# Performance work log

Hardware: AMD Instinct MI355X
Metric: run time of the kernel (lower is better)

Reference implementation:

```python
import jax, jax.numpy as jnp
import numpy as np

T, N, E = 12, 2048, 32768
X_DIM, H_DIM, Z_DIM, NL = 128, 256, 32, 2
EPS = 1e-10


def setup_inputs() -> dict:
    key = jax.random.key(0)
    ks = jax.random.split(key, 24)
    s = 0.1  # reset_parameters stdv
    p = {}
    p['x'] = jax.random.normal(ks[0], (T, N, X_DIM), jnp.float32)
    p['edge_index'] = jax.random.randint(ks[1], (T, 2, E), 0, N, dtype=jnp.int32)
    p['adj'] = (jax.random.uniform(ks[2], (T, N, N)) < 0.01).astype(jnp.float32)
    p['eps_src'] = jax.random.normal(ks[3], (T, N, Z_DIM), jnp.float32)
    p['eps_dst'] = jax.random.normal(ks[4], (T, N, Z_DIM), jnp.float32)
    p['phi_x_w'] = s * jax.random.normal(ks[5], (X_DIM, H_DIM), jnp.float32)
    p['phi_z_w'] = s * jax.random.normal(ks[6], (2 * Z_DIM, H_DIM), jnp.float32)
    p['gru_xw0'] = s * jax.random.normal(ks[7], (3, 2 * H_DIM, H_DIM), jnp.float32)  # (z,r,h) layer 0
    p['gru_xw1'] = s * jax.random.normal(ks[8], (3, H_DIM, H_DIM), jnp.float32)      # (z,r,h) layer 1
    p['gru_hw'] = s * jax.random.normal(ks[9], (NL, 3, H_DIM, H_DIM), jnp.float32)
    p['enc_w'] = s * jax.random.normal(ks[10], (2, 2 * H_DIM, H_DIM), jnp.float32)   # [src,dst]
    p['enc_b'] = s * jax.random.normal(ks[11], (2, H_DIM), jnp.float32)
    p['mean_w'] = s * jax.random.normal(ks[12], (2, H_DIM, Z_DIM), jnp.float32)
    p['mean_b'] = s * jax.random.normal(ks[13], (2, Z_DIM), jnp.float32)
    p['std_w'] = s * jax.random.normal(ks[14], (2, H_DIM, Z_DIM), jnp.float32)
    p['std_b'] = s * jax.random.normal(ks[15], (2, Z_DIM), jnp.float32)
    p['pri_w'] = s * jax.random.normal(ks[16], (2, H_DIM, H_DIM), jnp.float32)
    p['pri_b'] = s * jax.random.normal(ks[17], (2, H_DIM), jnp.float32)
    p['pri_mw'] = s * jax.random.normal(ks[18], (2, H_DIM, Z_DIM), jnp.float32)
    p['pri_mb'] = s * jax.random.normal(ks[19], (2, Z_DIM), jnp.float32)
    p['pri_sw'] = s * jax.random.normal(ks[20], (2, H_DIM, Z_DIM), jnp.float32)
    p['pri_sb'] = s * jax.random.normal(ks[21], (2, Z_DIM), jnp.float32)
    return p


def _gin_pre(x, src, dst):
    # GIN (eps=0): x + sum_{(src->dst)} x[src]; linear applied by caller
    return x + jax.ops.segment_sum(x[src], dst, num_segments=N)


def _gcn(x, w, b, src, dst):
    # GCNConv with self-loops and symmetric normalization
    deg = jax.ops.segment_sum(jnp.ones(src.shape[0], x.dtype), dst, num_segments=N) + 1.0
    dinv = deg ** -0.5
    nrm = dinv[src] * dinv[dst]
    xw = x @ w
    agg = jax.ops.segment_sum(nrm[:, None] * xw[src], dst, num_segments=N)
    return agg + xw / deg[:, None] + b


def _kld(m1, s1, m2, s2):
    k = (2 * jnp.log(s2 + EPS) - 2 * jnp.log(s1 + EPS)
         + ((s1 + EPS) ** 2 + (m1 - m2) ** 2) / (s2 + EPS) ** 2 - 1.0)
    return 0.5 / N * jnp.mean(jnp.sum(k, axis=1))


def reference(x, edge_index, adj, eps_src, eps_dst, phi_x_w, phi_z_w,
              gru_xw0, gru_xw1, gru_hw, enc_w, enc_b, mean_w, mean_b,
              std_w, std_b, pri_w, pri_b, pri_mw, pri_mb, pri_sw, pri_sb):
    h0 = jnp.zeros((NL, N, H_DIM), x.dtype)

    def step(h, inp):
        x_t, e_t, a_t, es_t, ed_t = inp
        src, dst = e_t[0], e_t[1]
        phi_x_t = jax.nn.relu(x_t @ phi_x_w)
        cat = jnp.concatenate([phi_x_t, h[-1]], axis=1)  # [N, 2H]
        cat_pre = _gin_pre(cat, src, dst)
        enc_s = jax.nn.relu(cat_pre @ enc_w[0] + enc_b[0])
        enc_d = jax.nn.relu(cat_pre @ enc_w[1] + enc_b[1])
        mean_s = _gcn(enc_s, mean_w[0], mean_b[0], src, dst)
        std_s = jax.nn.softplus(_gin_pre(enc_s, src, dst) @ std_w[0] + std_b[0])
        mean_d = _gcn(enc_d, mean_w[1], mean_b[1], src, dst)
        std_d = jax.nn.softplus(_gin_pre(enc_d, src, dst) @ std_w[1] + std_b[1])
        pri_s = jax.nn.relu(h[-1] @ pri_w[0] + pri_b[0])
        pm_s = pri_s @ pri_mw[0] + pri_mb[0]
        ps_s = jax.nn.softplus(pri_s @ pri_sw[0] + pri_sb[0])
        pri_d = jax.nn.relu(h[-1] @ pri_w[1] + pri_b[1])
        pm_d = pri_d @ pri_mw[1] + pri_mb[1]
        ps_d = jax.nn.softplus(pri_d @ pri_sw[1] + pri_sb[1])
        z_s = mean_s + std_s * es_t
        z_d = mean_d + std_d * ed_t
        phi_z_t = jax.nn.relu(jnp.concatenate([z_s, z_d], axis=1) @ phi_z_w)
        dec = z_s @ z_d.T  # [N, N] inner-product decoder (identity act)
        # graph-GRU across layers
        g_in = jnp.concatenate([phi_x_t, phi_z_t], axis=1)  # [N, 2H]
        new_h = []
        for i in range(NL):
            xi = g_in if i == 0 else new_h[i - 1]
            xw = gru_xw0 if i == 0 else gru_xw1
            xpre = _gin_pre(xi, src, dst)
            hpre = _gin_pre(h[i], src, dst)
            z_g = jax.nn.sigmoid(xpre @ xw[0] + hpre @ gru_hw[i, 0])
            r_g = jax.nn.sigmoid(xpre @ xw[1] + hpre @ gru_hw[i, 1])
            h_t = jnp.tanh(xpre @ xw[2] + _gin_pre(r_g * h[i], src, dst) @ gru_hw[i, 2])
            new_h.append(z_g * h[i] + (1.0 - z_g) * h_t)
        h_new = jnp.stack(new_h)
        kld = _kld(mean_s, std_s, pm_s, ps_s) + _kld(mean_d, std_d, pm_d, ps_d)
        ssum = a_t.sum()
        nn2 = jnp.asarray(N * N, a_t.dtype)
        posw = (nn2 - ssum) / ssum
        norm = nn2 / ((nn2 - ssum) * 2.0)
        bce = -posw * a_t * jax.nn.log_sigmoid(dec) - (1.0 - a_t) * jax.nn.log_sigmoid(-dec)
        nll = norm * jnp.mean(bce)
        return h_new, (kld, nll, dec)

    _, (klds, nlls, decs) = jax.lax.scan(step, h0, (x, edge_index, adj, eps_src, eps_dst))
    return jnp.sum(klds), jnp.sum(nlls), decs
```

## Files before the change

### kernel.cpp

```cpp
#include <hip/hip_runtime.h>
#include <math.h>

#define NTS 12
#define NND 2048
#define NED 32768
#define XDI 128
#define HDI 256
#define ZDI 32
#define EPSC 1e-10f
#define NH ((size_t)NND * HDI)
#define NZ ((size_t)NND * ZDI)
#define ZPL ((size_t)NND * 64)
#define XSZ ((size_t)NTS * NND * XDI)

typedef unsigned short u16;
typedef __bf16 bf16x8 __attribute__((ext_vector_type(8)));
typedef float f32x4 __attribute__((ext_vector_type(4)));

#define MF(a, b, c) __builtin_amdgcn_mfma_f32_16x16x32_bf16(a, b, c, 0, 0, 0)


__device__ __forceinline__ float lsigf(float x) {
    return fminf(x, 0.f) - log1pf(expf(-fabsf(x)));
}
__device__ __forceinline__ float splus(float v) {
    return fmaxf(v, 0.f) + log1pf(expf(-fabsf(v)));
}
__device__ __forceinline__ u16 f2b(float f) {
    unsigned u = __float_as_uint(f);
    u += 0x7fffu + ((u >> 16) & 1u);
    return (u16)(u >> 16);
}
__device__ __forceinline__ float b2f(u16 b) {
    return __uint_as_float((unsigned)b << 16);
}
__device__ __forceinline__ void f2b2(float v, u16& hi, u16& lo) {
    hi = f2b(v);
    lo = f2b(v - b2f(hi));
}
__device__ __forceinline__ void st_b16(u16* buf, size_t plane, size_t idx, float v) {
    u16 hi, lo;
    f2b2(v, hi, lo);
    buf[idx] = hi;
    buf[plane + idx] = lo;
}
__device__ __forceinline__ void st_b16v4(u16* buf, size_t plane, size_t idx, float4 v) {
    ushort4 h, l;
    f2b2(v.x, h.x, l.x); f2b2(v.y, h.y, l.y);
    f2b2(v.z, h.z, l.z); f2b2(v.w, h.w, l.w);
    *(ushort4*)(buf + idx) = h;
    *(ushort4*)(buf + plane + idx) = l;
}
__device__ __forceinline__ float4 ld_hl4(const u16* b, size_t plane, size_t idx) {
    ushort4 h = *(const ushort4*)(b + idx);
    ushort4 l = *(const ushort4*)(b + plane + idx);
    float4 r;
    r.x = b2f(h.x) + b2f(l.x); r.y = b2f(h.y) + b2f(l.y);
    r.z = b2f(h.z) + b2f(l.z); r.w = b2f(h.w) + b2f(l.w);
    return r;
}
__device__ float4 gin_hl(const u16* buf, size_t plane, int n, const int* __restrict__ offs,
                         const int* __restrict__ cs, int lane) {
    int e0 = offs[n], e1 = offs[n + 1];
    size_t c4 = (size_t)lane * 4;
    float4 a = ld_hl4(buf, plane, (size_t)n * HDI + c4);
    for (int j = e0; j < e1; j++) {
        float4 v = ld_hl4(buf, plane, (size_t)cs[j] * HDI + c4);
        a.x += v.x; a.y += v.y; a.z += v.z; a.w += v.w;
    }
    return a;
}

__host__ __device__ inline size_t wtoff(int m) {
    if (m == 0) return 0;
    if (m == 1) return 65536;
    return 98304 + (size_t)(m - 2) * 131072;
}

__device__ __forceinline__ void mm64(f32x4* A12, const u16* __restrict__ Ahi, size_t apl,
                                     const u16* __restrict__ Bt, int K,
                                     int row0, int cc, int lr, int kg) {
    const u16* bp = Bt + (size_t)(cc * 16 + lr) * K + kg;
    const u16* blp = bp + (size_t)K * HDI;
    const u16* ap0 = Ahi + (size_t)(row0 + lr) * K + kg;
    for (int k0 = 0; k0 < K; k0 += 32) {
        bf16x8 bh = *(const bf16x8*)(bp + k0);
        bf16x8 bl = *(const bf16x8*)(blp + k0);
#pragma unroll
        for (int s = 0; s < 4; s++) {
            const u16* ap = ap0 + (size_t)(16 * s) * K;
            bf16x8 ah = *(const bf16x8*)(ap + k0);
            bf16x8 al = *(const bf16x8*)(ap + apl + k0);
            A12[s * 3 + 0] = MF(ah, bh, A12[s * 3 + 0]);
            A12[s * 3 + 1] = MF(al, bh, A12[s * 3 + 1]);
            A12[s * 3 + 2] = MF(ah, bl, A12[s * 3 + 2]);
        }
    }
}

__device__ __forceinline__ void epi_hl(f32x4* A12, u16* dst, size_t plane,
                                       int row0, int cc, int lane, int relu) {
    int col = cc * 16 + (lane & 15);
    int rb0 = (lane >> 4) << 2;
#pragma unroll
    for (int s = 0; s < 4; s++)
#pragma unroll
        for (int i = 0; i < 4; i++) {
            int row = row0 + s * 16 + rb0 + i;
            float v = A12[s * 3][i] + A12[s * 3 + 1][i] + A12[s * 3 + 2][i];
            if (relu) v = fmaxf(v, 0.f);
            st_b16(dst, plane, (size_t)row * HDI + col, v);
        }
}


__global__ __launch_bounds__(256) void k0_setup(const int* __restrict__ ei,
                                                const float* __restrict__ x,
                                                const float* w_phix, const float* w_phiz,
                                                const float* w_enc, const float* w_pri,
                                                const float* w_gx0, const float* w_gx1,
                                                const float* w_gh,
                                                u16* __restrict__ warena, u16* __restrict__ xb,
                                                int* __restrict__ counts) {
    const int bid = blockIdx.x, tid = threadIdx.x;
    if (bid < 1536) {
        int idx = bid * 256 + tid;
        int t = idx >> 15, e = idx & (NED - 1);
        atomicAdd(&counts[t * NND + ei[(size_t)t * 2 * NED + NED + e]], 1);
    } else if (bid < 7424) {
        int u = bid - 1536;
        int m = u >> 8, k = u & 255;
        const int Kt = (m == 0) ? 128 : (m == 1) ? 64 : 256;
        if (k < Kt) {
            const int srcsel[23] = {0, 1, 2, 2, 2, 2, 3, 3, 4, 4, 4, 4,
                                    4, 4, 6, 6, 6, 5, 5, 5, 6, 6, 6};
            const int srcoff[23] = {0, 0, 0, 65536, 131072, 196608, 0, 65536,
                                    0, 65536, 131072, 196608, 262144, 327680,
                                    0, 65536, 131072, 0, 65536, 131072,
                                    196608, 262144, 327680};
            const float* srcs[7] = {w_phix, w_phiz, w_enc, w_pri, w_gx0, w_gx1, w_gh};
            const float* W = srcs[srcsel[m]] + srcoff[m];
            u16* D = warena + wtoff(m);
            float v = W[(size_t)k * 256 + tid];
            u16 hi, lo;
            f2b2(v, hi, lo);
            D[(size_t)tid * Kt + k] = hi;
            D[(size_t)Kt * 256 + (size_t)tid * Kt + k] = lo;
        }
    } else {
        size_t i = (size_t)(bid - 7424) * 256 + tid;
        float4 v = ((const float4*)x)[i];
        ushort4 h, l;
        f2b2(v.x, h.x, l.x); f2b2(v.y, h.y, l.y);
        f2b2(v.z, h.z, l.z); f2b2(v.w, h.w, l.w);
        ((ushort4*)xb)[i] = h;
        ((ushort4*)(xb + XSZ))[i] = l;
    }
}

__global__ __launch_bounds__(256) void k1_scan_phix(const int* __restrict__ counts,
                                                    int* __restrict__ offs,
                                                    float* __restrict__ deg,
                                                    float* __restrict__ dinv,
                                                    const u16* __restrict__ xb,
                                                    const u16* __restrict__ warena,
                                                    u16* __restrict__ phixb) {
    __shared__ int tsum[256];
    const int bid = blockIdx.x, tid = threadIdx.x;
    if (bid < 12) {
        const int* cnt = counts + bid * NND;
        int* off = offs + bid * (NND + 1);
        float* dg = deg + bid * NND;
        float* dv = dinv + bid * NND;
        int base = tid * 8;
        int local[8];
        int s = 0;
        for (int i = 0; i < 8; i++) { local[i] = s; s += cnt[base + i]; }
        tsum[tid] = s;
        __syncthreads();
        for (int o = 1; o < 256; o <<= 1) {
            int v = (tid >= o) ? tsum[tid - o] : 0;
            __syncthreads();
            tsum[tid] += v;
            __syncthreads();
        }
        int excl = tsum[tid] - s;
        for (int i = 0; i < 8; i++) off[base + i] = excl + local[i];
        if (tid == 255) off[NND] = excl + s;
        for (int i = 0; i < 8; i++) {
            float d = (float)cnt[base + i] + 1.0f;
            dg[base + i] = d;
            dv[base + i] = 1.0f / sqrtf(d);
        }
    } else {
        int u = bid - 12;
        int t = u >> 7, tile = u & 127;
        const int wid = tid >> 6, lane = tid & 63;
        const int lr = lane & 15, kg = (lane >> 4) * 8;
        int row0 = (tile >> 4) * 256 + wid * 64, cc = tile & 15;
        f32x4 A12[12] = {};
        mm64(A12, xb + (size_t)t * NND * XDI, XSZ, warena + wtoff(0), XDI, row0, cc, lr, kg);
        epi_hl(A12, phixb + (size_t)t * 2 * NH, NH, row0, cc, lane, 1);
    }
}

__global__ __launch_bounds__(256) void k2_fill(const int* __restrict__ ei,
                                               const int* __restrict__ offs,
                                               int* __restrict__ cursor,
                                               const float* __restrict__ dinv,
                                               int* __restrict__ csrc,
                                               float* __restrict__ csrw) {
    int idx = blockIdx.x * 256 + threadIdx.x;
    int t = idx >> 15, e = idx & (NED - 1);
    const int* src = ei + (size_t)t * 2 * NED;
    const int* dst = src + NED;
    int d = dst[e], s = src[e];
    const int* off_t = offs + t * (NND + 1);
    int pos = off_t[d] + atomicAdd(&cursor[t * NND + d], 1);
    csrc[(size_t)t * NED + pos] = s;
    csrw[(size_t)t * NED + pos] = dinv[t * NND + s] * dinv[t * NND + d];
}


__global__ __launch_bounds__(256) void kA(const u16* __restrict__ phxt,
                                          const u16* __restrict__ h1b,
                                          const u16* __restrict__ warena,
                                          u16* __restrict__ Ub, float* __restrict__ prif,
                                          const float* __restrict__ b_pri) {
    const int bid = blockIdx.x, tid = threadIdx.x;
    const int wid = tid >> 6, lane = tid & 63;
    const int lr = lane & 15, kg = (lane >> 4) * 8;
    f32x4 A12[12] = {};
    if (bid < 256) {
        int o = bid >> 7, tile = bid & 127;
        int row0 = (tile >> 4) * 256 + wid * 64, cc = tile & 15;
        mm64(A12, phxt, NH, warena + wtoff(2 + 2 * o), HDI, row0, cc, lr, kg);
        mm64(A12, h1b, NH, warena + wtoff(3 + 2 * o), HDI, row0, cc, lr, kg);
        epi_hl(A12, Ub + (size_t)o * 2 * NH, NH, row0, cc, lane, 0);
    } else {
        int q = bid - 256;
        int o = q >> 7, tile = q & 127;
        int row0 = (tile >> 4) * 256 + wid * 64, cc = tile & 15;
        mm64(A12, h1b, NH, warena + wtoff(6 + o), HDI, row0, cc, lr, kg);
        int col = cc * 16 + lr;
        int rb0 = (lane >> 4) << 2;
        float* C = prif + (size_t)o * NH;
        float bv = b_pri[o * HDI + col];
#pragma unroll
        for (int s = 0; s < 4; s++)
#pragma unroll
            for (int i = 0; i < 4; i++) {
                int row = row0 + s * 16 + rb0 + i;
                float v = A12[s * 3][i] + A12[s * 3 + 1][i] + A12[s * 3 + 2][i] + bv;
                C[(size_t)row * HDI + col] = fmaxf(v, 0.f);
            }
    }
}

__global__ __launch_bounds__(256) void kB(const u16* __restrict__ Ub,
                                          const float* __restrict__ prif,
                                          const int* __restrict__ offs,
                                          const int* __restrict__ cs,
                                          const float* __restrict__ b_enc,
                                          const float* __restrict__ w_mean,
                                          const float* __restrict__ w_std,
                                          const float* __restrict__ w_pm,
                                          const float* __restrict__ b_pm,
                                          const float* __restrict__ w_ps,
                                          const float* __restrict__ b_ps,
                                          float* __restrict__ xw, float* __restrict__ pmps) {
    __shared__ float rowbuf[4][256];
    const int tid = threadIdx.x;
    const int wid = tid >> 6, lane = tid & 63;
    const int u = blockIdx.x * 4 + wid;
    if (u < 4096) {
        int seg = u >> 11, n = u & 2047;
        float4 a = gin_hl(Ub + (size_t)seg * 2 * NH, NH, n, offs, cs, lane);
        const float* eb = b_enc + seg * HDI + lane * 4;
        a.x = fmaxf(a.x + eb[0], 0.f);
        a.y = fmaxf(a.y + eb[1], 0.f);
        a.z = fmaxf(a.z + eb[2], 0.f);
        a.w = fmaxf(a.w + eb[3], 0.f);
        *(float4*)&rowbuf[wid][lane * 4] = a;
        const float* B = ((lane < 32) ? w_mean : w_std) + seg * 8192;
        int m = lane & 31;
        float acc = 0.f;
        const float* rb = rowbuf[wid];
#pragma unroll 8
        for (int k = 0; k < 256; k++) acc += rb[k] * B[k * 32 + m];
        float* O = xw + ((lane < 32) ? seg : 2 + seg) * NZ;
        O[(size_t)n * ZDI + m] = acc;
    } else {
        int q = u - 4096;
        int s = q >> 10, unit = q & 1023;
        int n = unit * 2 + (lane >> 5);
        int m = lane & 31;
        const float* A = prif + ((s < 2) ? 0 : NH);
        const float* B = (s & 1) ? (w_ps + (s >> 1) * 8192) : (w_pm + (s >> 1) * 8192);
        const float* bi = (s & 1) ? (b_ps + (s >> 1) * 32) : (b_pm + (s >> 1) * 32);
        float acc = bi[m];
        const float* ar = A + (size_t)n * HDI;
#pragma unroll 4
        for (int k = 0; k < 256; k += 4) {
            float4 a4 = *(const float4*)(ar + k);
            acc += a4.x * B[(k + 0) * 32 + m];
            acc += a4.y * B[(k + 1) * 32 + m];
            acc += a4.z * B[(k + 2) * 32 + m];
            acc += a4.w * B[(k + 3) * 32 + m];
        }
        if (s & 1) acc = splus(acc);
        pmps[(size_t)s * NZ + (size_t)n * ZDI + m] = acc;
    }
}

__global__ __launch_bounds__(256) void kC(const float* __restrict__ xw,
                                          const float* __restrict__ pmps,
                                          const int* __restrict__ offs,
                                          const int* __restrict__ cs,
                                          const float* __restrict__ cw,
                                          const float* __restrict__ dgv,
                                          const float* __restrict__ b_mean,
                                          const float* __restrict__ b_std,
                                          const float* __restrict__ es,
                                          const float* __restrict__ ed,
                                          float* __restrict__ zcatf, u16* __restrict__ zcatb,
                                          double* __restrict__ accd) {
    __shared__ double smd[4];
    const int tid = threadIdx.x;
    const int wid = tid >> 6, lane = tid & 63;
    const int n = blockIdx.x * 4 + wid;
    const int sel = lane >> 5, m = lane & 31;
    const float* xwm = xw + sel * NZ;
    const float* xws = xw + (2 + sel) * NZ;
    int e0 = offs[n], e1 = offs[n + 1];
    float am = 0.f, as_ = xws[(size_t)n * ZDI + m];
    for (int j = e0; j < e1; j++) {
        int s = cs[j];
        am += cw[j] * xwm[(size_t)s * ZDI + m];
        as_ += xws[(size_t)s * ZDI + m];
    }
    float mean = am + xwm[(size_t)n * ZDI + m] / dgv[n] + b_mean[sel * 32 + m];
    float sd = splus(as_ + b_std[sel * 32 + m]);
    const float* eps = sel ? ed : es;
    float z = mean + sd * eps[(size_t)n * ZDI + m];
    size_t zi = (size_t)n * 64 + sel * 32 + m;
    zcatf[zi] = z;
    st_b16(zcatb, ZPL, zi, z);
    float pm = pmps[(size_t)(sel * 2) * NZ + (size_t)n * ZDI + m];
    float ps = pmps[(size_t)(sel * 2 + 1) * NZ + (size_t)n * ZDI + m];
    float a1v = sd + EPSC, a2v = ps + EPSC;
    float dm = mean - pm;
    double kl = (double)(2.f * (logf(a2v) - logf(a1v)) +
                         (a1v * a1v + dm * dm) / (a2v * a2v) - 1.f);
#pragma unroll
    for (int o = 32; o > 0; o >>= 1) kl += __shfl_down(kl, o);
    if (lane == 0) smd[wid] = kl;
    __syncthreads();
    if (tid == 0) atomicAdd(accd, smd[0] + smd[1] + smd[2] + smd[3]);
}

__global__ __launch_bounds__(256) void kD(const float* __restrict__ zcatf,
                                          const u16* __restrict__ zcatb,
                                          const float* __restrict__ adjt,
                                          const u16* __restrict__ warena,
                                          float* __restrict__ dect,
                                          u16* __restrict__ phizb,
                                          double* __restrict__ bcet) {
    __shared__ float smf[2 * 32 * 68];
    const int bid = blockIdx.x, tid = threadIdx.x;
    if (bid < 1024) {
        float (*zsS)[68] = (float(*)[68])smf;
        float (*zdS)[68] = (float(*)[68])(smf + 32 * 68);
        const int tx = tid & 15, ty = tid >> 4;
        const int c0 = (bid & 31) * 64, r0 = (bid >> 5) * 64;
        const int lrow = tid >> 2;
        const int lk = (tid & 3) * 8;
        float4 v0 = *(const float4*)&zcatf[(size_t)(r0 + lrow) * 64 + lk];
        float4 v1 = *(const float4*)&zcatf[(size_t)(r0 + lrow) * 64 + lk + 4];
        float4 w0 = *(const float4*)&zcatf[(size_t)(c0 + lrow) * 64 + 32 + lk];
        float4 w1 = *(const float4*)&zcatf[(size_t)(c0 + lrow) * 64 + 32 + lk + 4];
        zsS[lk + 0][lrow] = v0.x; zsS[lk + 1][lrow] = v0.y; zsS[lk + 2][lrow] = v0.z; zsS[lk + 3][lrow] = v0.w;
        zsS[lk + 4][lrow] = v1.x; zsS[lk + 5][lrow] = v1.y; zsS[lk + 6][lrow] = v1.z; zsS[lk + 7][lrow] = v1.w;
        zdS[lk + 0][lrow] = w0.x; zdS[lk + 1][lrow] = w0.y; zdS[lk + 2][lrow] = w0.z; zdS[lk + 3][lrow] = w0.w;
        zdS[lk + 4][lrow] = w1.x; zdS[lk + 5][lrow] = w1.y; zdS[lk + 6][lrow] = w1.z; zdS[lk + 7][lrow] = w1.w;
        __syncthreads();

        float acc[4][4] = {};
#pragma unroll
        for (int k = 0; k < 32; k++) {
            const float4 a4 = *(const float4*)&zsS[k][ty * 4];
            const float4 b4 = *(const float4*)&zdS[k][tx * 4];
            const float aa[4] = {a4.x, a4.y, a4.z, a4.w};
            const float bb[4] = {b4.x, b4.y, b4.z, b4.w};
#pragma unroll
            for (int i = 0; i < 4; i++)
#pragma unroll
                for (int j = 0; j < 4; j++) acc[i][j] += aa[i] * bb[j];
        }

        float pa = 0.f, p1 = 0.f, p2 = 0.f;
#pragma unroll
        for (int i = 0; i < 4; i++) {
            const int r = r0 + ty * 4 + i;
            const float4 av4 = *(const float4*)&adjt[(size_t)r * NND + c0 + tx * 4];
            const float av[4] = {av4.x, av4.y, av4.z, av4.w};
            float* drow = &dect[(size_t)r * NND + c0 + tx * 4];
#pragma unroll
            for (int j = 0; j < 4; j++) {
                float d = acc[i][j];
                __builtin_nontemporal_store(d, &drow[j]);
                float a = av[j];
                pa += a;
                p1 += a * lsigf(d);
                p2 += (1.f - a) * lsigf(-d);
            }
        }
        __syncthreads();
        smf[tid] = pa; smf[256 + tid] = p1; smf[512 + tid] = p2;
        __syncthreads();
        for (int o = 128; o > 0; o >>= 1) {
            if (tid < o) {
                smf[tid] += smf[tid + o];
                smf[256 + tid] += smf[256 + tid + o];
                smf[512 + tid] += smf[512 + tid + o];
            }
            __syncthreads();
        }
        if (tid == 0) {
            double* b = bcet + (size_t)bid * 3;
            b[0] = (double)smf[0];
            b[1] = (double)smf[256];
            b[2] = (double)smf[512];
        }
    } else {
        int u = bid - 1024;
        const int wid = tid >> 6, lane = tid & 63;
        const int lr = lane & 15, kg = (lane >> 4) * 8;
        int row0 = (u >> 4) * 256 + wid * 64, cc = u & 15;
        f32x4 A12[12] = {};
        mm64(A12, zcatb, ZPL, warena + wtoff(1), 64, row0, cc, lr, kg);
        epi_hl(A12, phizb, NH, row0, cc, lane, 1);
    }
}

__global__ __launch_bounds__(256) void kE(const u16* __restrict__ phxt,
                                          const u16* __restrict__ phizb,
                                          const u16* __restrict__ h0b,
                                          const u16* __restrict__ warena,
                                          u16* __restrict__ Pb) {
    const int bid = blockIdx.x, tid = threadIdx.x;
    const int wid = tid >> 6, lane = tid & 63;
    const int lr = lane & 15, kg = (lane >> 4) * 8;
    int o = bid >> 7, tile = bid & 127;
    int row0 = (tile >> 4) * 256 + wid * 64, cc = tile & 15;
    f32x4 A12[12] = {};
    if (o == 0) {
        mm64(A12, phxt, NH, warena + wtoff(8), HDI, row0, cc, lr, kg);
        mm64(A12, phizb, NH, warena + wtoff(9), HDI, row0, cc, lr, kg);
        mm64(A12, h0b, NH, warena + wtoff(14), HDI, row0, cc, lr, kg);
    } else if (o == 1) {
        mm64(A12, phxt, NH, warena + wtoff(10), HDI, row0, cc, lr, kg);
        mm64(A12, phizb, NH, warena + wtoff(11), HDI, row0, cc, lr, kg);
        mm64(A12, h0b, NH, warena + wtoff(15), HDI, row0, cc, lr, kg);
    } else {
        mm64(A12, phxt, NH, warena + wtoff(12), HDI, row0, cc, lr, kg);
        mm64(A12, phizb, NH, warena + wtoff(13), HDI, row0, cc, lr, kg);
    }
    epi_hl(A12, Pb + (size_t)o * 2 * NH, NH, row0, cc, lane, 0);
}

__global__ __launch_bounds__(256) void kE1(const u16* __restrict__ nh0b,
                                           const u16* __restrict__ h1b,
                                           const u16* __restrict__ warena,
                                           u16* __restrict__ Pb) {
    const int bid = blockIdx.x, tid = threadIdx.x;
    const int wid = tid >> 6, lane = tid & 63;
    const int lr = lane & 15, kg = (lane >> 4) * 8;
    int o = bid >> 7, tile = bid & 127;
    int row0 = (tile >> 4) * 256 + wid * 64, cc = tile & 15;
    f32x4 A12[12] = {};
    if (o == 0) {
        mm64(A12, nh0b, NH, warena + wtoff(17), HDI, row0, cc, lr, kg);
        mm64(A12, h1b, NH, warena + wtoff(20), HDI, row0, cc, lr, kg);
    } else if (o == 1) {
        mm64(A12, nh0b, NH, warena + wtoff(18), HDI, row0, cc, lr, kg);
        mm64(A12, h1b, NH, warena + wtoff(21), HDI, row0, cc, lr, kg);
    } else {
        mm64(A12, nh0b, NH, warena + wtoff(19), HDI, row0, cc, lr, kg);
    }
    epi_hl(A12, Pb + (size_t)o * 2 * NH, NH, row0, cc, lane, 0);
}

__global__ __launch_bounds__(256) void kF(const u16* __restrict__ Pb,
                                          const u16* __restrict__ hb,
                                          float* __restrict__ zGf, u16* __restrict__ rhb,
                                          const int* __restrict__ offs,
                                          const int* __restrict__ cs) {
    const int tid = threadIdx.x;
    const int wid = tid >> 6, lane = tid & 63;
    const int u = blockIdx.x * 4 + wid;
    int seg = u >> 11, n = u & 2047;
    size_t idx = (size_t)n * HDI + lane * 4;
    if (seg == 0) {
        float4 a = gin_hl(Pb, NH, n, offs, cs, lane);
        a.x = 1.f / (1.f + expf(-a.x)); a.y = 1.f / (1.f + expf(-a.y));
        a.z = 1.f / (1.f + expf(-a.z)); a.w = 1.f / (1.f + expf(-a.w));
        *(float4*)&zGf[idx] = a;
    } else {
        float4 a = gin_hl(Pb + 2 * NH, NH, n, offs, cs, lane);
        float4 h4 = ld_hl4(hb, NH, idx);
        float4 rh;
        rh.x = h4.x / (1.f + expf(-a.x)); rh.y = h4.y / (1.f + expf(-a.y));
        rh.z = h4.z / (1.f + expf(-a.z)); rh.w = h4.w / (1.f + expf(-a.w));
        st_b16v4(rhb, NH, idx, rh);
    }
}

__global__ __launch_bounds__(256) void kG(const u16* __restrict__ rhb,
                                          const u16* __restrict__ warena, int wtm,
                                          const u16* __restrict__ Pb, u16* __restrict__ Rb) {
    const int bid = blockIdx.x, tid = threadIdx.x;
    const int wid = tid >> 6, lane = tid & 63;
    const int lr = lane & 15, kg = (lane >> 4) * 8;
    int row0 = (bid >> 4) * 256 + wid * 64, cc = bid & 15;
    f32x4 A12[12] = {};
    mm64(A12, rhb, NH, warena + wtoff(wtm), HDI, row0, cc, lr, kg);
    const u16* Ph = Pb + 4 * NH;
    int col = cc * 16 + lr;
    int rb0 = (lane >> 4) << 2;
#pragma unroll
    for (int s = 0; s < 4; s++)
#pragma unroll
        for (int i = 0; i < 4; i++) {
            int row = row0 + s * 16 + rb0 + i;
            size_t idx = (size_t)row * HDI + col;
            float v = A12[s * 3][i] + A12[s * 3 + 1][i] + A12[s * 3 + 2][i] +
                      b2f(Ph[idx]) + b2f(Ph[NH + idx]);
            st_b16(Rb, NH, idx, v);
        }
}

__global__ __launch_bounds__(256) void kH(const u16* __restrict__ Rb,
                                          const float* __restrict__ zGf,
                                          const u16* __restrict__ hb,
                                          u16* __restrict__ nhb,
                                          const int* __restrict__ offs,
                                          const int* __restrict__ cs) {
    const int tid = threadIdx.x;
    const int wid = tid >> 6, lane = tid & 63;
    const int n = blockIdx.x * 4 + wid;
    size_t idx = (size_t)n * HDI + lane * 4;
    float4 a = gin_hl(Rb, NH, n, offs, cs, lane);
    float4 z4 = *(const float4*)&zGf[idx];
    float4 h4 = ld_hl4(hb, NH, idx);
    float4 o;
    o.x = z4.x * h4.x + (1.f - z4.x) * tanhf(a.x);
    o.y = z4.y * h4.y + (1.f - z4.y) * tanhf(a.y);
    o.z = z4.z * h4.z + (1.f - z4.z) * tanhf(a.z);
    o.w = z4.w * h4.w + (1.f - z4.w) * tanhf(a.w);
    st_b16v4(nhb, NH, idx, o);
}

__global__ __launch_bounds__(256) void kFin(const double* __restrict__ accd,
                                            const double* __restrict__ bce,
                                            float* __restrict__ out) {
    __shared__ double red[256];
    __shared__ double sums[36];
    const int tid = threadIdx.x;
    for (int p = 0; p < 36; p++) {
        int t = p / 3, c = p % 3;
        double s = 0.0;
        for (int i = tid; i < 1024; i += 256) s += bce[((size_t)t * 1024 + i) * 3 + c];
        red[tid] = s;
        __syncthreads();
        for (int o = 128; o > 0; o >>= 1) {
            if (tid < o) red[tid] += red[tid + o];
            __syncthreads();
        }
        if (tid == 0) sums[p] = red[0];
        __syncthreads();
    }
    if (tid == 0) {
        const double nn2 = (double)NND * (double)NND;
        out[0] = (float)(0.5 * accd[0] / nn2);
        double nll = 0.0;
        for (int t = 0; t < NTS; ++t) {
            double s = sums[t * 3 + 0];
            double S1 = sums[t * 3 + 1];
            double S2 = sums[t * 3 + 2];
            double posw = (nn2 - s) / s;
            double norm = nn2 / ((nn2 - s) * 2.0);
            nll += norm * (-posw * S1 - S2) / nn2;
        }
        out[1] = (float)nll;
    }
}


extern "C" void kernel_launch(void* const* d_in, const int* in_sizes, int n_in,
                              void* d_out, int out_size, void* d_ws, size_t ws_size,
                              hipStream_t stream) {
    (void)in_sizes; (void)n_in; (void)out_size; (void)ws_size;

    const float* x_all = (const float*)d_in[0];
    const int* ei_all = (const int*)d_in[1];
    const float* adj_all = (const float*)d_in[2];
    const float* eps_s_all = (const float*)d_in[3];
    const float* eps_d_all = (const float*)d_in[4];
    const float* phi_x_w = (const float*)d_in[5];
    const float* phi_z_w = (const float*)d_in[6];
    const float* gru_xw0 = (const float*)d_in[7];
    const float* gru_xw1 = (const float*)d_in[8];
    const float* gru_hw = (const float*)d_in[9];
    const float* enc_w = (const float*)d_in[10];
    const float* enc_b = (const float*)d_in[11];
    const float* mean_w = (const float*)d_in[12];
    const float* mean_b = (const float*)d_in[13];
    const float* std_w = (const float*)d_in[14];
    const float* std_b = (const float*)d_in[15];
    const float* pri_w = (const float*)d_in[16];
    const float* pri_b = (const float*)d_in[17];
    const float* pri_mw = (const float*)d_in[18];
    const float* pri_mb = (const float*)d_in[19];
    const float* pri_sw = (const float*)d_in[20];
    const float* pri_sb = (const float*)d_in[21];
    float* out = (float*)d_out;

    size_t off = 0;
    auto alloc = [&](size_t bytes) -> void* {
        void* p = (char*)d_ws + off;
        off = (off + bytes + 255) & ~(size_t)255;
        return p;
    };

    u16* warena = (u16*)alloc(2850816 * 2);
    u16* xb = (u16*)alloc(2 * XSZ * 2);
    u16* phixb = (u16*)alloc((size_t)NTS * 2 * NH * 2);
    u16* hbuf = (u16*)alloc(8 * NH * 2);
    u16* Ub = (u16*)alloc(4 * NH * 2);
    float* prif = (float*)alloc(2 * NH * 4);
    float* xw = (float*)alloc(4 * NZ * 4);
    float* pmps = (float*)alloc(4 * NZ * 4);
    float* zcatf = (float*)alloc(ZPL * 4);
    u16* zcatb = (u16*)alloc(2 * ZPL * 2);
    u16* phizb = (u16*)alloc(2 * NH * 2);
    u16* Pb = (u16*)alloc(6 * NH * 2);
    float* zGf = (float*)alloc(NH * 4);
    u16* rhb = (u16*)alloc(2 * NH * 2);
    u16* Rb = (u16*)alloc(2 * NH * 2);
    float* deg = (float*)alloc((size_t)NTS * NND * 4);
    float* dinv = (float*)alloc((size_t)NTS * NND * 4);
    int* counts = (int*)alloc(2 * (size_t)NTS * NND * 4);
    int* cursor = counts + (size_t)NTS * NND;
    int* offs = (int*)alloc((size_t)NTS * (NND + 1) * 4);
    int* csrc = (int*)alloc((size_t)NTS * NED * 4);
    float* csrw = (float*)alloc((size_t)NTS * NED * 4);
    double* accd = (double*)alloc(8 * 8);
    double* bce = (double*)alloc((size_t)NTS * 1024 * 3 * 8);

    u16* h0b[2] = {hbuf, hbuf + 2 * NH};
    u16* h1b[2] = {hbuf + 4 * NH, hbuf + 6 * NH};

    hipMemsetAsync(hbuf, 0, 8 * NH * 2, stream);
    hipMemsetAsync(counts, 0, 2 * (size_t)NTS * NND * 4, stream);
    hipMemsetAsync(accd, 0, 8 * 8, stream);

    k0_setup<<<10496, 256, 0, stream>>>(ei_all, x_all, phi_x_w, phi_z_w, enc_w, pri_w,
                                        gru_xw0, gru_xw1, gru_hw, warena, xb, counts);
    k1_scan_phix<<<12 + 1536, 256, 0, stream>>>(counts, offs, deg, dinv, xb, warena, phixb);
    k2_fill<<<1536, 256, 0, stream>>>(ei_all, offs, cursor, dinv, csrc, csrw);

    for (int t = 0; t < NTS; ++t) {
        const int cur = t & 1;
        const int* off_t = offs + (size_t)t * (NND + 1);
        const int* cs_t = csrc + (size_t)t * NED;
        const float* cw_t = csrw + (size_t)t * NED;
        const float* dg_t = deg + (size_t)t * NND;
        const u16* phxt = phixb + (size_t)t * 2 * NH;
        const float* adj_t = adj_all + (size_t)t * NND * NND;
        float* dec_t = out + 2 + (size_t)t * NND * NND;
        const float* es_t = eps_s_all + (size_t)t * NZ;
        const float* ed_t = eps_d_all + (size_t)t * NZ;
        double* bce_t = bce + (size_t)t * 1024 * 3;

        kA<<<512, 256, 0, stream>>>(phxt, h1b[cur], warena, Ub, prif, pri_b);
        kB<<<2048, 256, 0, stream>>>(Ub, prif, off_t, cs_t, enc_b, mean_w, std_w,
                                     pri_mw, pri_mb, pri_sw, pri_sb, xw, pmps);
        kC<<<512, 256, 0, stream>>>(xw, pmps, off_t, cs_t, cw_t, dg_t, mean_b, std_b,
                                    es_t, ed_t, zcatf, zcatb, accd);
        kD<<<1152, 256, 0, stream>>>(zcatf, zcatb, adj_t, warena, dec_t, phizb, bce_t);
        kE<<<384, 256, 0, stream>>>(phxt, phizb, h0b[cur], warena, Pb);
        kF<<<1024, 256, 0, stream>>>(Pb, h0b[cur], zGf, rhb, off_t, cs_t);
        kG<<<128, 256, 0, stream>>>(rhb, warena, 16, Pb, Rb);
        kH<<<512, 256, 0, stream>>>(Rb, zGf, h0b[cur], h0b[cur ^ 1], off_t, cs_t);
        kE1<<<384, 256, 0, stream>>>(h0b[cur ^ 1], h1b[cur], warena, Pb);
        kF<<<1024, 256, 0, stream>>>(Pb, h1b[cur], zGf, rhb, off_t, cs_t);
        kG<<<128, 256, 0, stream>>>(rhb, warena, 22, Pb, Rb);
        kH<<<512, 256, 0, stream>>>(Rb, zGf, h1b[cur], h1b[cur ^ 1], off_t, cs_t);
    }

    kFin<<<1, 256, 0, stream>>>(accd, bce, out);
}
```

Measured before the change: 3.408 ms.

## Fuse per-timestep GRU/encoder/prior stages into fewer 16-row LDS-staged kernels

Restructures the per-timestep pipeline from twelve launches into about five. The GEMMs now work on 16-row tiles that stage intermediates such as z, phi_z and the new h in LDS as hi/lo bf16 planes, which removes global round-trips and several small kernels. The next step's encoder and prior GEMMs are computed in the previous step's final kernel (kHA), and the decoder is merged with kF/kG. The layer-1 GRU update is skipped on the last timestep, which is safe only because h_new from the final step is never output. The cost is fewer blocks (128) on the fused kernels, so occupancy is lower and B-matrix reuse is poorer.

Result: slower. 6.880 ms (+101.9%).

```diff
diff --git a/kernel.cpp b/kernel.cpp
--- a/kernel.cpp
+++ b/kernel.cpp
@@ -12,6 +12,10 @@
 #define NZ ((size_t)NND * ZDI)
 #define ZPL ((size_t)NND * 64)
 #define XSZ ((size_t)NTS * NND * XDI)
+#define LSTR 264
+#define LPH (16 * 264)
+#define LSZ 72
+#define LPZ (16 * 72)
 
 typedef unsigned short u16;
 typedef __bf16 bf16x8 __attribute__((ext_vector_type(8)));
@@ -77,39 +81,71 @@
     return 98304 + (size_t)(m - 2) * 131072;
 }
 
-__device__ __forceinline__ void mm64(f32x4* A12, const u16* __restrict__ Ahi, size_t apl,
-                                     const u16* __restrict__ Bt, int K,
-                                     int row0, int cc, int lr, int kg) {
-    const u16* bp = Bt + (size_t)(cc * 16 + lr) * K + kg;
-    const u16* blp = bp + (size_t)K * HDI;
-    const u16* ap0 = Ahi + (size_t)(row0 + lr) * K + kg;
+__device__ __forceinline__ void mmg16(f32x4* a12, const u16* __restrict__ Ahi, size_t apl,
+                                      int n0, const u16* __restrict__ Bt,
+                                      int ctbase, int lr, int kg) {
+    const int K = 256;
+    const u16* ap = Ahi + (size_t)(n0 + lr) * K + kg;
+    for (int k0 = 0; k0 < 256; k0 += 32) {
+        bf16x8 ah = *(const bf16x8*)(ap + k0);
+        bf16x8 al = *(const bf16x8*)(ap + apl + k0);
+#pragma unroll
+        for (int ct = 0; ct < 4; ct++) {
+            const u16* bp = Bt + (size_t)((ctbase + ct) * 16 + lr) * K + kg + k0;
+            bf16x8 bh = *(const bf16x8*)bp;
+            bf16x8 bl = *(const bf16x8*)(bp + (size_t)K * HDI);
+            a12[ct * 3 + 0] = MF(ah, bh, a12[ct * 3 + 0]);
+            a12[ct * 3 + 1] = MF(al, bh, a12[ct * 3 + 1]);
+            a12[ct * 3 + 2] = MF(ah, bl, a12[ct * 3 + 2]);
+        }
+    }
+}
+__device__ __forceinline__ void mml16(f32x4* a12, const u16* lds, int S, int LP,
+                                      const u16* __restrict__ Bt, int K,
+                                      int ctbase, int lr, int kg) {
     for (int k0 = 0; k0 < K; k0 += 32) {
-        bf16x8 bh = *(const bf16x8*)(bp + k0);
-        bf16x8 bl = *(const bf16x8*)(blp + k0);
-#pragma unroll
-        for (int s = 0; s < 4; s++) {
-            const u16* ap = ap0 + (size_t)(16 * s) * K;
-            bf16x8 ah = *(const bf16x8*)(ap + k0);
-            bf16x8 al = *(const bf16x8*)(ap + apl + k0);
-            A12[s * 3 + 0] = MF(ah, bh, A12[s * 3 + 0]);
-            A12[s * 3 + 1] = MF(al, bh, A12[s * 3 + 1]);
-            A12[s * 3 + 2] = MF(ah, bl, A12[s * 3 + 2]);
-        }
-    }
-}
-
-__device__ __forceinline__ void epi_hl(f32x4* A12, u16* dst, size_t plane,
-                                       int row0, int cc, int lane, int relu) {
-    int col = cc * 16 + (lane & 15);
-    int rb0 = (lane >> 4) << 2;
-#pragma unroll
-    for (int s = 0; s < 4; s++)
+        bf16x8 ah = *(const bf16x8*)(lds + lr * S + kg + k0);
+        bf16x8 al = *(const bf16x8*)(lds + LP + lr * S + kg + k0);
+#pragma unroll
+        for (int ct = 0; ct < 4; ct++) {
+            const u16* bp = Bt + (size_t)((ctbase + ct) * 16 + lr) * K + kg + k0;
+            bf16x8 bh = *(const bf16x8*)bp;
+            bf16x8 bl = *(const bf16x8*)(bp + (size_t)K * HDI);
+            a12[ct * 3 + 0] = MF(ah, bh, a12[ct * 3 + 0]);
+            a12[ct * 3 + 1] = MF(al, bh, a12[ct * 3 + 1]);
+            a12[ct * 3 + 2] = MF(ah, bl, a12[ct * 3 + 2]);
+        }
+    }
+}
+__device__ __forceinline__ void epi16_hl(f32x4* a12, u16* dst, int n0, int ctbase,
+                                         int lane, int relu) {
+    int lr = lane & 15, rb0 = (lane >> 4) * 4;
+#pragma unroll
+    for (int ct = 0; ct < 4; ct++)
 #pragma unroll
         for (int i = 0; i < 4; i++) {
-            int row = row0 + s * 16 + rb0 + i;
-            float v = A12[s * 3][i] + A12[s * 3 + 1][i] + A12[s * 3 + 2][i];
+            int row = n0 + rb0 + i;
+            int col = (ctbase + ct) * 16 + lr;
+            float v = a12[ct * 3][i] + a12[ct * 3 + 1][i] + a12[ct * 3 + 2][i];
             if (relu) v = fmaxf(v, 0.f);
-            st_b16(dst, plane, (size_t)row * HDI + col, v);
+            st_b16(dst, NH, (size_t)row * HDI + col, v);
+        }
+}
+__device__ __forceinline__ void epi16_lds(f32x4* a12, u16* lds, int S, int LP,
+                                          int ctbase, int lane, int relu) {
+    int lr = lane & 15, rb0 = (lane >> 4) * 4;
+#pragma unroll
+    for (int ct = 0; ct < 4; ct++)
+#pragma unroll
+        for (int i = 0; i < 4; i++) {
+            int rl = rb0 + i;
+            int col = (ctbase + ct) * 16 + lr;
+            float v = a12[ct * 3][i] + a12[ct * 3 + 1][i] + a12[ct * 3 + 2][i];
+            if (relu) v = fmaxf(v, 0.f);
+            u16 hi, lo;
+            f2b2(v, hi, lo);
+            lds[rl * S + col] = hi;
+            lds[LP + rl * S + col] = lo;
         }
 }
 
@@ -197,10 +233,32 @@
         int t = u >> 7, tile = u & 127;
         const int wid = tid >> 6, lane = tid & 63;
         const int lr = lane & 15, kg = (lane >> 4) * 8;
-        int row0 = (tile >> 4) * 256 + wid * 64, cc = tile & 15;
-        f32x4 A12[12] = {};
-        mm64(A12, xb + (size_t)t * NND * XDI, XSZ, warena + wtoff(0), XDI, row0, cc, lr, kg);
-        epi_hl(A12, phixb + (size_t)t * 2 * NH, NH, row0, cc, lane, 1);
+        int n0 = (tile >> 4) * 256 + wid * 64;
+        int cc = tile & 15;
+        const u16* A = xb + (size_t)t * NND * XDI;
+        u16* dst = phixb + (size_t)t * 2 * NH;
+#pragma unroll
+        for (int s = 0; s < 4; s++) {
+            int rbase = n0 + s * 16;
+            f32x4 a3[3] = {};
+            const u16* ap = A + (size_t)(rbase + lr) * XDI + kg;
+            const u16* bp = warena + wtoff(0) + (size_t)(cc * 16 + lr) * XDI + kg;
+            for (int k0 = 0; k0 < XDI; k0 += 32) {
+                bf16x8 ah = *(const bf16x8*)(ap + k0);
+                bf16x8 al = *(const bf16x8*)(ap + XSZ + k0);
+                bf16x8 bh = *(const bf16x8*)(bp + k0);
+                bf16x8 bl = *(const bf16x8*)(bp + (size_t)XDI * HDI + k0);
+                a3[0] = MF(ah, bh, a3[0]);
+                a3[1] = MF(al, bh, a3[1]);
+                a3[2] = MF(ah, bl, a3[2]);
+            }
+            int col = cc * 16 + lr, rb0 = (lane >> 4) * 4;
+#pragma unroll
+            for (int i = 0; i < 4; i++) {
+                float v = fmaxf(a3[0][i] + a3[1][i] + a3[2][i], 0.f);
+                st_b16(dst, NH, (size_t)(rbase + rb0 + i) * HDI + col, v);
+            }
+        }
     }
 }
 
@@ -222,95 +280,33 @@
 }
 
 
-__global__ __launch_bounds__(256) void kA(const u16* __restrict__ phxt,
-                                          const u16* __restrict__ h1b,
-                                          const u16* __restrict__ warena,
-                                          u16* __restrict__ Ub, float* __restrict__ prif,
-                                          const float* __restrict__ b_pri) {
-    const int bid = blockIdx.x, tid = threadIdx.x;
-    const int wid = tid >> 6, lane = tid & 63;
-    const int lr = lane & 15, kg = (lane >> 4) * 8;
-    f32x4 A12[12] = {};
-    if (bid < 256) {
-        int o = bid >> 7, tile = bid & 127;
-        int row0 = (tile >> 4) * 256 + wid * 64, cc = tile & 15;
-        mm64(A12, phxt, NH, warena + wtoff(2 + 2 * o), HDI, row0, cc, lr, kg);
-        mm64(A12, h1b, NH, warena + wtoff(3 + 2 * o), HDI, row0, cc, lr, kg);
-        epi_hl(A12, Ub + (size_t)o * 2 * NH, NH, row0, cc, lane, 0);
-    } else {
-        int q = bid - 256;
-        int o = q >> 7, tile = q & 127;
-        int row0 = (tile >> 4) * 256 + wid * 64, cc = tile & 15;
-        mm64(A12, h1b, NH, warena + wtoff(6 + o), HDI, row0, cc, lr, kg);
-        int col = cc * 16 + lr;
-        int rb0 = (lane >> 4) << 2;
-        float* C = prif + (size_t)o * NH;
-        float bv = b_pri[o * HDI + col];
-#pragma unroll
-        for (int s = 0; s < 4; s++)
-#pragma unroll
-            for (int i = 0; i < 4; i++) {
-                int row = row0 + s * 16 + rb0 + i;
-                float v = A12[s * 3][i] + A12[s * 3 + 1][i] + A12[s * 3 + 2][i] + bv;
-                C[(size_t)row * HDI + col] = fmaxf(v, 0.f);
-            }
-    }
-}
-
 __global__ __launch_bounds__(256) void kB(const u16* __restrict__ Ub,
-                                          const float* __restrict__ prif,
                                           const int* __restrict__ offs,
                                           const int* __restrict__ cs,
                                           const float* __restrict__ b_enc,
                                           const float* __restrict__ w_mean,
                                           const float* __restrict__ w_std,
-                                          const float* __restrict__ w_pm,
-                                          const float* __restrict__ b_pm,
-                                          const float* __restrict__ w_ps,
-                                          const float* __restrict__ b_ps,
-                                          float* __restrict__ xw, float* __restrict__ pmps) {
+                                          float* __restrict__ xw) {
     __shared__ float rowbuf[4][256];
     const int tid = threadIdx.x;
     const int wid = tid >> 6, lane = tid & 63;
     const int u = blockIdx.x * 4 + wid;
-    if (u < 4096) {
-        int seg = u >> 11, n = u & 2047;
-        float4 a = gin_hl(Ub + (size_t)seg * 2 * NH, NH, n, offs, cs, lane);
-        const float* eb = b_enc + seg * HDI + lane * 4;
-        a.x = fmaxf(a.x + eb[0], 0.f);
-        a.y = fmaxf(a.y + eb[1], 0.f);
-        a.z = fmaxf(a.z + eb[2], 0.f);
-        a.w = fmaxf(a.w + eb[3], 0.f);
-        *(float4*)&rowbuf[wid][lane * 4] = a;
-        const float* B = ((lane < 32) ? w_mean : w_std) + seg * 8192;
-        int m = lane & 31;
-        float acc = 0.f;
-        const float* rb = rowbuf[wid];
+    int seg = u >> 11, n = u & 2047;
+    float4 a = gin_hl(Ub + (size_t)seg * 2 * NH, NH, n, offs, cs, lane);
+    const float* eb = b_enc + seg * HDI + lane * 4;
+    a.x = fmaxf(a.x + eb[0], 0.f);
+    a.y = fmaxf(a.y + eb[1], 0.f);
+    a.z = fmaxf(a.z + eb[2], 0.f);
+    a.w = fmaxf(a.w + eb[3], 0.f);
+    *(float4*)&rowbuf[wid][lane * 4] = a;
+    const float* B = ((lane < 32) ? w_mean : w_std) + seg * 8192;
+    int m = lane & 31;
+    float acc = 0.f;
+    const float* rb = rowbuf[wid];
 #pragma unroll 8
-        for (int k = 0; k < 256; k++) acc += rb[k] * B[k * 32 + m];
-        float* O = xw + ((lane < 32) ? seg : 2 + seg) * NZ;
-        O[(size_t)n * ZDI + m] = acc;
-    } else {
-        int q = u - 4096;
-        int s = q >> 10, unit = q & 1023;
-        int n = unit * 2 + (lane >> 5);
-        int m = lane & 31;
-        const float* A = prif + ((s < 2) ? 0 : NH);
-        const float* B = (s & 1) ? (w_ps + (s >> 1) * 8192) : (w_pm + (s >> 1) * 8192);
-        const float* bi = (s & 1) ? (b_ps + (s >> 1) * 32) : (b_pm + (s >> 1) * 32);
-        float acc = bi[m];
-        const float* ar = A + (size_t)n * HDI;
-#pragma unroll 4
-        for (int k = 0; k < 256; k += 4) {
-            float4 a4 = *(const float4*)(ar + k);
-            acc += a4.x * B[(k + 0) * 32 + m];
-            acc += a4.y * B[(k + 1) * 32 + m];
-            acc += a4.z * B[(k + 2) * 32 + m];
-            acc += a4.w * B[(k + 3) * 32 + m];
-        }
-        if (s & 1) acc = splus(acc);
-        pmps[(size_t)s * NZ + (size_t)n * ZDI + m] = acc;
-    }
+    for (int k = 0; k < 256; k++) acc += rb[k] * B[k * 32 + m];
+    float* O = xw + ((lane < 32) ? seg : 2 + seg) * NZ;
+    O[(size_t)n * ZDI + m] = acc;
 }
 
 __global__ __launch_bounds__(256) void kC(const float* __restrict__ xw,
@@ -323,35 +319,65 @@
                                           const float* __restrict__ b_std,
                                           const float* __restrict__ es,
                                           const float* __restrict__ ed,
-                                          float* __restrict__ zcatf, u16* __restrict__ zcatb,
+                                          float* __restrict__ zcatf,
+                                          const u16* __restrict__ phx,
+                                          const u16* __restrict__ h0,
+                                          const u16* __restrict__ warena,
+                                          u16* __restrict__ Pb,
                                           double* __restrict__ accd) {
+    __shared__ __align__(16) u16 lz[2 * 16 * 72];
+    __shared__ __align__(16) u16 lp[2 * 16 * 264];
     __shared__ double smd[4];
-    const int tid = threadIdx.x;
+    const int tid = threadIdx.x, bid = blockIdx.x;
     const int wid = tid >> 6, lane = tid & 63;
-    const int n = blockIdx.x * 4 + wid;
+    const int lr = lane & 15, kg = (lane >> 4) * 8;
+    const int n0 = bid * 16;
     const int sel = lane >> 5, m = lane & 31;
-    const float* xwm = xw + sel * NZ;
-    const float* xws = xw + (2 + sel) * NZ;
-    int e0 = offs[n], e1 = offs[n + 1];
-    float am = 0.f, as_ = xws[(size_t)n * ZDI + m];
-    for (int j = e0; j < e1; j++) {
-        int s = cs[j];
-        am += cw[j] * xwm[(size_t)s * ZDI + m];
-        as_ += xws[(size_t)s * ZDI + m];
-    }
-    float mean = am + xwm[(size_t)n * ZDI + m] / dgv[n] + b_mean[sel * 32 + m];
-    float sd = splus(as_ + b_std[sel * 32 + m]);
-    const float* eps = sel ? ed : es;
-    float z = mean + sd * eps[(size_t)n * ZDI + m];
-    size_t zi = (size_t)n * 64 + sel * 32 + m;
-    zcatf[zi] = z;
-    st_b16(zcatb, ZPL, zi, z);
-    float pm = pmps[(size_t)(sel * 2) * NZ + (size_t)n * ZDI + m];
-    float ps = pmps[(size_t)(sel * 2 + 1) * NZ + (size_t)n * ZDI + m];
-    float a1v = sd + EPSC, a2v = ps + EPSC;
-    float dm = mean - pm;
-    double kl = (double)(2.f * (logf(a2v) - logf(a1v)) +
-                         (a1v * a1v + dm * dm) / (a2v * a2v) - 1.f);
+    const float* xwm = xw + (size_t)sel * NZ;
+    const float* xws = xw + (size_t)(2 + sel) * NZ;
+    double kl = 0.0;
+    for (int rr = 0; rr < 4; rr++) {
+        int rl = wid * 4 + rr, n = n0 + rl;
+        int e0 = offs[n], e1 = offs[n + 1];
+        float am = 0.f, as_ = xws[(size_t)n * ZDI + m];
+        for (int j = e0; j < e1; j++) {
+            int s = cs[j];
+            am += cw[j] * xwm[(size_t)s * ZDI + m];
+            as_ += xws[(size_t)s * ZDI + m];
+        }
+        float mean = am + xwm[(size_t)n * ZDI + m] / dgv[n] + b_mean[sel * 32 + m];
+        float sd = splus(as_ + b_std[sel * 32 + m]);
+        const float* eps = sel ? ed : es;
+        float z = mean + sd * eps[(size_t)n * ZDI + m];
+        zcatf[(size_t)n * 64 + sel * 32 + m] = z;
+        u16 hi, lo;
+        f2b2(z, hi, lo);
+        lz[rl * LSZ + sel * 32 + m] = hi;
+        lz[LPZ + rl * LSZ + sel * 32 + m] = lo;
+        float pm = pmps[(size_t)(sel * 2) * NZ + (size_t)n * ZDI + m];
+        float ps = pmps[(size_t)(sel * 2 + 1) * NZ + (size_t)n * ZDI + m];
+        float a1v = sd + EPSC, a2v = ps + EPSC;
+        float dm = mean - pm;
+        kl += (double)(2.f * (logf(a2v) - logf(a1v)) +
+                       (a1v * a1v + dm * dm) / (a2v * a2v) - 1.f);
+    }
+    __syncthreads();
+    {
+        f32x4 a12[12] = {};
+        mml16(a12, lz, LSZ, LPZ, warena + wtoff(1), 64, wid * 4, lr, kg);
+        epi16_lds(a12, lp, LSTR, LPH, wid * 4, lane, 1);
+    }
+    __syncthreads();
+    {
+        const int wA[3] = {8, 10, 12}, wB[3] = {9, 11, 13}, wH[3] = {14, 15, 0};
+        for (int g = 0; g < 3; g++) {
+            f32x4 a12[12] = {};
+            mmg16(a12, phx, NH, n0, warena + wtoff(wA[g]), wid * 4, lr, kg);
+            mml16(a12, lp, LSTR, LPH, warena + wtoff(wB[g]), 256, wid * 4, lr, kg);
+            if (g < 2) mmg16(a12, h0, NH, n0, warena + wtoff(wH[g]), wid * 4, lr, kg);
+            epi16_hl(a12, Pb + (size_t)g * 2 * NH, n0, wid * 4, lane, 0);
+        }
+    }
 #pragma unroll
     for (int o = 32; o > 0; o >>= 1) kl += __shfl_down(kl, o);
     if (lane == 0) smd[wid] = kl;
@@ -359,20 +385,66 @@
     if (tid == 0) atomicAdd(accd, smd[0] + smd[1] + smd[2] + smd[3]);
 }
 
-__global__ __launch_bounds__(256) void kD(const float* __restrict__ zcatf,
-                                          const u16* __restrict__ zcatb,
-                                          const float* __restrict__ adjt,
-                                          const u16* __restrict__ warena,
-                                          float* __restrict__ dect,
-                                          u16* __restrict__ phizb,
-                                          double* __restrict__ bcet) {
-    __shared__ float smf[2 * 32 * 68];
+__global__ __launch_bounds__(256) void kFG(const u16* __restrict__ Pb,
+                                           const u16* __restrict__ hb,
+                                           const u16* __restrict__ warena, int wtm,
+                                           float* __restrict__ zGf, u16* __restrict__ Rb,
+                                           const int* __restrict__ offs,
+                                           const int* __restrict__ cs,
+                                           const float* __restrict__ zcatf,
+                                           const float* __restrict__ adjt,
+                                           float* __restrict__ dect,
+                                           double* __restrict__ bcet) {
+    __shared__ __align__(16) char smem[17408];
     const int bid = blockIdx.x, tid = threadIdx.x;
-    if (bid < 1024) {
+    if (bid < 128) {
+        u16* lrh = (u16*)smem;
+        const int wid = tid >> 6, lane = tid & 63;
+        const int lr = lane & 15, kg = (lane >> 4) * 8;
+        const int n0 = bid * 16;
+        const int c4 = lane * 4;
+        for (int rr = 0; rr < 4; rr++) {
+            int rl = wid * 4 + rr, n = n0 + rl;
+            size_t idx = (size_t)n * HDI + c4;
+            float4 az = gin_hl(Pb, NH, n, offs, cs, lane);
+            float4 zg;
+            zg.x = 1.f / (1.f + expf(-az.x)); zg.y = 1.f / (1.f + expf(-az.y));
+            zg.z = 1.f / (1.f + expf(-az.z)); zg.w = 1.f / (1.f + expf(-az.w));
+            *(float4*)&zGf[idx] = zg;
+            float4 ar = gin_hl(Pb + 2 * NH, NH, n, offs, cs, lane);
+            float4 h4 = ld_hl4(hb, NH, idx);
+            float4 rh;
+            rh.x = h4.x / (1.f + expf(-ar.x)); rh.y = h4.y / (1.f + expf(-ar.y));
+            rh.z = h4.z / (1.f + expf(-ar.z)); rh.w = h4.w / (1.f + expf(-ar.w));
+            ushort4 hh, ll;
+            f2b2(rh.x, hh.x, ll.x); f2b2(rh.y, hh.y, ll.y);
+            f2b2(rh.z, hh.z, ll.z); f2b2(rh.w, hh.w, ll.w);
+            *(ushort4*)(lrh + rl * LSTR + c4) = hh;
+            *(ushort4*)(lrh + LPH + rl * LSTR + c4) = ll;
+        }
+        __syncthreads();
+        f32x4 a12[12] = {};
+        mml16(a12, lrh, LSTR, LPH, warena + wtoff(wtm), 256, wid * 4, lr, kg);
+        const u16* Ph = Pb + 4 * NH;
+        int rb0 = (lane >> 4) * 4;
+#pragma unroll
+        for (int ct = 0; ct < 4; ct++)
+#pragma unroll
+            for (int i = 0; i < 4; i++) {
+                int row = n0 + rb0 + i;
+                int col = (wid * 4 + ct) * 16 + lr;
+                size_t idx = (size_t)row * HDI + col;
+                float v = a12[ct * 3][i] + a12[ct * 3 + 1][i] + a12[ct * 3 + 2][i] +
+                          b2f(Ph[idx]) + b2f(Ph[NH + idx]);
+                st_b16(Rb, NH, idx, v);
+            }
+    } else {
+        float* smf = (float*)smem;
+        const int db = bid - 128;
         float (*zsS)[68] = (float(*)[68])smf;
         float (*zdS)[68] = (float(*)[68])(smf + 32 * 68);
         const int tx = tid & 15, ty = tid >> 4;
-        const int c0 = (bid & 31) * 64, r0 = (bid >> 5) * 64;
+        const int c0 = (db & 31) * 64, r0 = (db >> 5) * 64;
         const int lrow = tid >> 2;
         const int lk = (tid & 3) * 8;
         float4 v0 = *(const float4*)&zcatf[(size_t)(r0 + lrow) * 64 + lk];
@@ -427,138 +499,141 @@
             __syncthreads();
         }
         if (tid == 0) {
-            double* b = bcet + (size_t)bid * 3;
+            double* b = bcet + (size_t)db * 3;
             b[0] = (double)smf[0];
             b[1] = (double)smf[256];
             b[2] = (double)smf[512];
         }
-    } else {
-        int u = bid - 1024;
-        const int wid = tid >> 6, lane = tid & 63;
-        const int lr = lane & 15, kg = (lane >> 4) * 8;
-        int row0 = (u >> 4) * 256 + wid * 64, cc = u & 15;
-        f32x4 A12[12] = {};
-        mm64(A12, zcatb, ZPL, warena + wtoff(1), 64, row0, cc, lr, kg);
-        epi_hl(A12, phizb, NH, row0, cc, lane, 1);
-    }
-}
-
-__global__ __launch_bounds__(256) void kE(const u16* __restrict__ phxt,
-                                          const u16* __restrict__ phizb,
-                                          const u16* __restrict__ h0b,
-                                          const u16* __restrict__ warena,
-                                          u16* __restrict__ Pb) {
-    const int bid = blockIdx.x, tid = threadIdx.x;
+    }
+}
+
+__global__ __launch_bounds__(256) void kHE1(const u16* __restrict__ Rb,
+                                            const float* __restrict__ zGf,
+                                            const u16* __restrict__ h0c,
+                                            u16* __restrict__ h0n,
+                                            const u16* __restrict__ h1c,
+                                            const u16* __restrict__ warena,
+                                            u16* __restrict__ Pb,
+                                            const int* __restrict__ offs,
+                                            const int* __restrict__ cs) {
+    __shared__ __align__(16) u16 lnh[2 * 16 * 264];
+    const int tid = threadIdx.x, bid = blockIdx.x;
     const int wid = tid >> 6, lane = tid & 63;
     const int lr = lane & 15, kg = (lane >> 4) * 8;
-    int o = bid >> 7, tile = bid & 127;
-    int row0 = (tile >> 4) * 256 + wid * 64, cc = tile & 15;
-    f32x4 A12[12] = {};
-    if (o == 0) {
-        mm64(A12, phxt, NH, warena + wtoff(8), HDI, row0, cc, lr, kg);
-        mm64(A12, phizb, NH, warena + wtoff(9), HDI, row0, cc, lr, kg);
-        mm64(A12, h0b, NH, warena + wtoff(14), HDI, row0, cc, lr, kg);
-    } else if (o == 1) {
-        mm64(A12, phxt, NH, warena + wtoff(10), HDI, row0, cc, lr, kg);
-        mm64(A12, phizb, NH, warena + wtoff(11), HDI, row0, cc, lr, kg);
-        mm64(A12, h0b, NH, warena + wtoff(15), HDI, row0, cc, lr, kg);
-    } else {
-        mm64(A12, phxt, NH, warena + wtoff(12), HDI, row0, cc, lr, kg);
-        mm64(A12, phizb, NH, warena + wtoff(13), HDI, row0, cc, lr, kg);
-    }
-    epi_hl(A12, Pb + (size_t)o * 2 * NH, NH, row0, cc, lane, 0);
-}
-
-__global__ __launch_bounds__(256) void kE1(const u16* __restrict__ nh0b,
-                                           const u16* __restrict__ h1b,
+    const int n0 = bid * 16;
+    const int c4 = lane * 4;
+    for (int rr = 0; rr < 4; rr++) {
+        int rl = wid * 4 + rr, n = n0 + rl;
+        size_t idx = (size_t)n * HDI + c4;
+        float4 a = gin_hl(Rb, NH, n, offs, cs, lane);
+        float4 z4 = *(const float4*)&zGf[idx];
+        float4 h4 = ld_hl4(h0c, NH, idx);
+        float4 o;
+        o.x = z4.x * h4.x + (1.f - z4.x) * tanhf(a.x);
+        o.y = z4.y * h4.y + (1.f - z4.y) * tanhf(a.y);
+        o.z = z4.z * h4.z + (1.f - z4.z) * tanhf(a.z);
+        o.w = z4.w * h4.w + (1.f - z4.w) * tanhf(a.w);
+        st_b16v4(h0n, NH, idx, o);
+        ushort4 hh, ll;
+        f2b2(o.x, hh.x, ll.x); f2b2(o.y, hh.y, ll.y);
+        f2b2(o.z, hh.z, ll.z); f2b2(o.w, hh.w, ll.w);
+        *(ushort4*)(lnh + rl * LSTR + c4) = hh;
+        *(ushort4*)(lnh + LPH + rl * LSTR + c4) = ll;
+    }
+    __syncthreads();
+    const int wN[3] = {17, 18, 19}, wH[3] = {20, 21, 0};
+    for (int g = 0; g < 3; g++) {
+        f32x4 a12[12] = {};
+        mml16(a12, lnh, LSTR, LPH, warena + wtoff(wN[g]), 256, wid * 4, lr, kg);
+        if (g < 2) mmg16(a12, h1c, NH, n0, warena + wtoff(wH[g]), wid * 4, lr, kg);
+        epi16_hl(a12, Pb + (size_t)g * 2 * NH, n0, wid * 4, lane, 0);
+    }
+}
+
+__global__ __launch_bounds__(256) void kHA(const u16* __restrict__ Rb,
+                                           const float* __restrict__ zGf,
+                                           const u16* __restrict__ h1c,
+                                           u16* __restrict__ h1n,
+                                           const u16* __restrict__ phxn,
                                            const u16* __restrict__ warena,
-                                           u16* __restrict__ Pb) {
-    const int bid = blockIdx.x, tid = threadIdx.x;
+                                           u16* __restrict__ Ub,
+                                           float* __restrict__ pmps,
+                                           const float* __restrict__ b_pri,
+                                           const float* __restrict__ w_pm,
+                                           const float* __restrict__ b_pm,
+                                           const float* __restrict__ w_ps,
+                                           const float* __restrict__ b_ps,
+                                           const int* __restrict__ offs,
+                                           const int* __restrict__ cs, int prep) {
+    __shared__ __align__(16) u16 lnh[2 * 16 * 264];
+    __shared__ __align__(16) float lpr[16 * 260];
+    const int tid = threadIdx.x, bid = blockIdx.x;
     const int wid = tid >> 6, lane = tid & 63;
     const int lr = lane & 15, kg = (lane >> 4) * 8;
-    int o = bid >> 7, tile = bid & 127;
-    int row0 = (tile >> 4) * 256 + wid * 64, cc = tile & 15;
-    f32x4 A12[12] = {};
-    if (o == 0) {
-        mm64(A12, nh0b, NH, warena + wtoff(17), HDI, row0, cc, lr, kg);
-        mm64(A12, h1b, NH, warena + wtoff(20), HDI, row0, cc, lr, kg);
-    } else if (o == 1) {
-        mm64(A12, nh0b, NH, warena + wtoff(18), HDI, row0, cc, lr, kg);
-        mm64(A12, h1b, NH, warena + wtoff(21), HDI, row0, cc, lr, kg);
+    const int n0 = bid * 16;
+    const int c4 = lane * 4;
+    if (prep) {
+        for (int i = tid; i < 2 * 16 * 264; i += 256) lnh[i] = 0;
     } else {
-        mm64(A12, nh0b, NH, warena + wtoff(19), HDI, row0, cc, lr, kg);
-    }
-    epi_hl(A12, Pb + (size_t)o * 2 * NH, NH, row0, cc, lane, 0);
-}
-
-__global__ __launch_bounds__(256) void kF(const u16* __restrict__ Pb,
-                                          const u16* __restrict__ hb,
-                                          float* __restrict__ zGf, u16* __restrict__ rhb,
-                                          const int* __restrict__ offs,
-                                          const int* __restrict__ cs) {
-    const int tid = threadIdx.x;
-    const int wid = tid >> 6, lane = tid & 63;
-    const int u = blockIdx.x * 4 + wid;
-    int seg = u >> 11, n = u & 2047;
-    size_t idx = (size_t)n * HDI + lane * 4;
-    if (seg == 0) {
-        float4 a = gin_hl(Pb, NH, n, offs, cs, lane);
-        a.x = 1.f / (1.f + expf(-a.x)); a.y = 1.f / (1.f + expf(-a.y));
-        a.z = 1.f / (1.f + expf(-a.z)); a.w = 1.f / (1.f + expf(-a.w));
-        *(float4*)&zGf[idx] = a;
-    } else {
-        float4 a = gin_hl(Pb + 2 * NH, NH, n, offs, cs, lane);
-        float4 h4 = ld_hl4(hb, NH, idx);
-        float4 rh;
-        rh.x = h4.x / (1.f + expf(-a.x)); rh.y = h4.y / (1.f + expf(-a.y));
-        rh.z = h4.z / (1.f + expf(-a.z)); rh.w = h4.w / (1.f + expf(-a.w));
-        st_b16v4(rhb, NH, idx, rh);
-    }
-}
-
-__global__ __launch_bounds__(256) void kG(const u16* __restrict__ rhb,
-                                          const u16* __restrict__ warena, int wtm,
-                                          const u16* __restrict__ Pb, u16* __restrict__ Rb) {
-    const int bid = blockIdx.x, tid = threadIdx.x;
-    const int wid = tid >> 6, lane = tid & 63;
-    const int lr = lane & 15, kg = (lane >> 4) * 8;
-    int row0 = (bid >> 4) * 256 + wid * 64, cc = bid & 15;
-    f32x4 A12[12] = {};
-    mm64(A12, rhb, NH, warena + wtoff(wtm), HDI, row0, cc, lr, kg);
-    const u16* Ph = Pb + 4 * NH;
-    int col = cc * 16 + lr;
-    int rb0 = (lane >> 4) << 2;
-#pragma unroll
-    for (int s = 0; s < 4; s++)
-#pragma unroll
-        for (int i = 0; i < 4; i++) {
-            int row = row0 + s * 16 + rb0 + i;
-            size_t idx = (size_t)row * HDI + col;
-            float v = A12[s * 3][i] + A12[s * 3 + 1][i] + A12[s * 3 + 2][i] +
-                      b2f(Ph[idx]) + b2f(Ph[NH + idx]);
-            st_b16(Rb, NH, idx, v);
-        }
-}
-
-__global__ __launch_bounds__(256) void kH(const u16* __restrict__ Rb,
-                                          const float* __restrict__ zGf,
-                                          const u16* __restrict__ hb,
-                                          u16* __restrict__ nhb,
-                                          const int* __restrict__ offs,
-                                          const int* __restrict__ cs) {
-    const int tid = threadIdx.x;
-    const int wid = tid >> 6, lane = tid & 63;
-    const int n = blockIdx.x * 4 + wid;
-    size_t idx = (size_t)n * HDI + lane * 4;
-    float4 a = gin_hl(Rb, NH, n, offs, cs, lane);
-    float4 z4 = *(const float4*)&zGf[idx];
-    float4 h4 = ld_hl4(hb, NH, idx);
-    float4 o;
-    o.x = z4.x * h4.x + (1.f - z4.x) * tanhf(a.x);
-    o.y = z4.y * h4.y + (1.f - z4.y) * tanhf(a.y);
-    o.z = z4.z * h4.z + (1.f - z4.z) * tanhf(a.z);
-    o.w = z4.w * h4.w + (1.f - z4.w) * tanhf(a.w);
-    st_b16v4(nhb, NH, idx, o);
+        for (int rr = 0; rr < 4; rr++) {
+            int rl = wid * 4 + rr, n = n0 + rl;
+            size_t idx = (size_t)n * HDI + c4;
+            float4 a = gin_hl(Rb, NH, n, offs, cs, lane);
+            float4 z4 = *(const float4*)&zGf[idx];
+            float4 h4 = ld_hl4(h1c, NH, idx);
+            float4 o;
+            o.x = z4.x * h4.x + (1.f - z4.x) * tanhf(a.x);
+            o.y = z4.y * h4.y + (1.f - z4.y) * tanhf(a.y);
+            o.z = z4.z * h4.z + (1.f - z4.z) * tanhf(a.z);
+            o.w = z4.w * h4.w + (1.f - z4.w) * tanhf(a.w);
+            st_b16v4(h1n, NH, idx, o);
+            ushort4 hh, ll;
+            f2b2(o.x, hh.x, ll.x); f2b2(o.y, hh.y, ll.y);
+            f2b2(o.z, hh.z, ll.z); f2b2(o.w, hh.w, ll.w);
+            *(ushort4*)(lnh + rl * LSTR + c4) = hh;
+            *(ushort4*)(lnh + LPH + rl * LSTR + c4) = ll;
+        }
+    }
+    __syncthreads();
+    for (int seg = 0; seg < 2; seg++) {
+        f32x4 a12[12] = {};
+        mmg16(a12, phxn, NH, n0, warena + wtoff(2 + 2 * seg), wid * 4, lr, kg);
+        mml16(a12, lnh, LSTR, LPH, warena + wtoff(3 + 2 * seg), 256, wid * 4, lr, kg);
+        epi16_hl(a12, Ub + (size_t)seg * 2 * NH, n0, wid * 4, lane, 0);
+    }
+    for (int seg = 0; seg < 2; seg++) {
+        {
+            f32x4 a12[12] = {};
+            mml16(a12, lnh, LSTR, LPH, warena + wtoff(6 + seg), 256, wid * 4, lr, kg);
+            int rb0 = (lane >> 4) * 4;
+#pragma unroll
+            for (int ct = 0; ct < 4; ct++)
+#pragma unroll
+                for (int i = 0; i < 4; i++) {
+                    int rl = rb0 + i;
+                    int col = (wid * 4 + ct) * 16 + lr;
+                    float v = a12[ct * 3][i] + a12[ct * 3 + 1][i] + a12[ct * 3 + 2][i] +
+                              b_pri[seg * HDI + col];
+                    lpr[rl * 260 + col] = fmaxf(v, 0.f);
+                }
+        }
+        __syncthreads();
+        {
+            int row_l = tid >> 4, q = tid & 15;
+#pragma unroll
+            for (int i = 0; i < 4; i++) {
+                int o = q * 4 + i;
+                int pl = o >> 5, mm = o & 31;
+                const float* w = (pl ? w_ps : w_pm) + seg * 8192;
+                float acc = (pl ? b_ps : b_pm)[seg * 32 + mm];
+                const float* pr = &lpr[row_l * 260];
+                for (int k = 0; k < 256; k++) acc += pr[k] * w[k * 32 + mm];
+                if (pl) acc = splus(acc);
+                pmps[(size_t)(seg * 2 + pl) * NZ + (size_t)(n0 + row_l) * ZDI + mm] = acc;
+            }
+        }
+        __syncthreads();
+    }
 }
 
 __global__ __launch_bounds__(256) void kFin(const double* __restrict__ accd,
@@ -638,15 +713,11 @@
     u16* phixb = (u16*)alloc((size_t)NTS * 2 * NH * 2);
     u16* hbuf = (u16*)alloc(8 * NH * 2);
     u16* Ub = (u16*)alloc(4 * NH * 2);
-    float* prif = (float*)alloc(2 * NH * 4);
     float* xw = (float*)alloc(4 * NZ * 4);
     float* pmps = (float*)alloc(4 * NZ * 4);
     float* zcatf = (float*)alloc(ZPL * 4);
-    u16* zcatb = (u16*)alloc(2 * ZPL * 2);
-    u16* phizb = (u16*)alloc(2 * NH * 2);
     u16* Pb = (u16*)alloc(6 * NH * 2);
     float* zGf = (float*)alloc(NH * 4);
-    u16* rhb = (u16*)alloc(2 * NH * 2);
     u16* Rb = (u16*)alloc(2 * NH * 2);
     float* deg = (float*)alloc((size_t)NTS * NND * 4);
     float* dinv = (float*)alloc((size_t)NTS * NND * 4);
@@ -669,6 +740,8 @@
                                         gru_xw0, gru_xw1, gru_hw, warena, xb, counts);
     k1_scan_phix<<<12 + 1536, 256, 0, stream>>>(counts, offs, deg, dinv, xb, warena, phixb);
     k2_fill<<<1536, 256, 0, stream>>>(ei_all, offs, cursor, dinv, csrc, csrw);
+    kHA<<<128, 256, 0, stream>>>(Rb, zGf, h1b[0], h1b[0], phixb, warena, Ub, pmps,
+                                 pri_b, pri_mw, pri_mb, pri_sw, pri_sb, offs, csrc, 1);
 
     for (int t = 0; t < NTS; ++t) {
         const int cur = t & 1;
@@ -683,20 +756,21 @@
         const float* ed_t = eps_d_all + (size_t)t * NZ;
         double* bce_t = bce + (size_t)t * 1024 * 3;
 
-        kA<<<512, 256, 0, stream>>>(phxt, h1b[cur], warena, Ub, prif, pri_b);
-        kB<<<2048, 256, 0, stream>>>(Ub, prif, off_t, cs_t, enc_b, mean_w, std_w,
-                                     pri_mw, pri_mb, pri_sw, pri_sb, xw, pmps);
-        kC<<<512, 256, 0, stream>>>(xw, pmps, off_t, cs_t, cw_t, dg_t, mean_b, std_b,
-                                    es_t, ed_t, zcatf, zcatb, accd);
-        kD<<<1152, 256, 0, stream>>>(zcatf, zcatb, adj_t, warena, dec_t, phizb, bce_t);
-        kE<<<384, 256, 0, stream>>>(phxt, phizb, h0b[cur], warena, Pb);
-        kF<<<1024, 256, 0, stream>>>(Pb, h0b[cur], zGf, rhb, off_t, cs_t);
-        kG<<<128, 256, 0, stream>>>(rhb, warena, 16, Pb, Rb);
-        kH<<<512, 256, 0, stream>>>(Rb, zGf, h0b[cur], h0b[cur ^ 1], off_t, cs_t);
-        kE1<<<384, 256, 0, stream>>>(h0b[cur ^ 1], h1b[cur], warena, Pb);
-        kF<<<1024, 256, 0, stream>>>(Pb, h1b[cur], zGf, rhb, off_t, cs_t);
-        kG<<<128, 256, 0, stream>>>(rhb, warena, 22, Pb, Rb);
-        kH<<<512, 256, 0, stream>>>(Rb, zGf, h1b[cur], h1b[cur ^ 1], off_t, cs_t);
+        kB<<<1024, 256, 0, stream>>>(Ub, off_t, cs_t, enc_b, mean_w, std_w, xw);
+        kC<<<128, 256, 0, stream>>>(xw, pmps, off_t, cs_t, cw_t, dg_t, mean_b, std_b,
+                                    es_t, ed_t, zcatf, phxt, h0b[cur], warena, Pb, accd);
+        kFG<<<1152, 256, 0, stream>>>(Pb, h0b[cur], warena, 16, zGf, Rb, off_t, cs_t,
+                                      zcatf, adj_t, dec_t, bce_t);
+        if (t < NTS - 1) {
+            kHE1<<<128, 256, 0, stream>>>(Rb, zGf, h0b[cur], h0b[cur ^ 1], h1b[cur],
+                                          warena, Pb, off_t, cs_t);
+            kFG<<<128, 256, 0, stream>>>(Pb, h1b[cur], warena, 22, zGf, Rb, off_t, cs_t,
+                                         zcatf, adj_t, dec_t, bce_t);
+            kHA<<<128, 256, 0, stream>>>(Rb, zGf, h1b[cur], h1b[cur ^ 1],
+                                         phixb + (size_t)(t + 1) * 2 * NH, warena, Ub, pmps,
+                                         pri_b, pri_mw, pri_mb, pri_sw, pri_sb,
+                                         off_t, cs_t, 0);
+        }
     }
 
     kFin<<<1, 256, 0, stream>>>(accd, bce, out);
```
